# Kernel tuning notes

Measured on AMD Instinct MI355X. Metric: run time of the kernel, lower is better.

## Reference

```python
import jax, jax.numpy as jnp
import numpy as np

B, S, D, L = 2, 1024, 1024, 48
K = max(1, int(L * 0.1))  # = 4, matches torch k = max(1, int(num_paths * 0.1))
EPS = 1e-5  # torch LayerNorm default


def setup_inputs() -> dict:
    key = jax.random.key(0)
    ks = jax.random.split(key, 7)
    inv = 1.0 / np.sqrt(D).astype(np.float32)
    return {
        "x": jax.random.normal(ks[0], (B, S, D), jnp.float32),
        "gate_w": jax.random.normal(ks[1], (L, D), jnp.float32) * inv,          # gate_proj weight [L,D], no bias
        "lattice_weights": jax.random.normal(ks[2], (L, D, D), jnp.float32) * 0.02,
        "out_w": jax.random.normal(ks[3], (D, D), jnp.float32) * inv,            # out_proj weight [D,D]
        "out_b": jnp.zeros((D,), jnp.float32),
        "ln_g": jnp.ones((D,), jnp.float32),
        "ln_b": jnp.zeros((D,), jnp.float32),
    }


def reference(x, gate_w, lattice_weights, out_w, out_b, ln_g, ln_b):
    # Gate: top-k routing over L lattice paths
    logits = jnp.einsum('bsd,ld->bsl', x, gate_w)                 # [B,S,L]
    top_vals, idx = jax.lax.top_k(logits, K)                      # [B,S,K] each (descending, like torch.topk)
    scores = jax.nn.softmax(top_vals, axis=-1)                    # [B,S,K]

    # Mathematically identical to gathering [B,S,K,D,D] expert matrices and
    # weight-summing, but computed as one dense GEMM over all L experts
    # followed by a cheap gather -- avoids the 32GB intermediate.
    out_all = jnp.einsum('bsd,lde->bsle', x, lattice_weights)     # [B,S,L,D]
    sel = jnp.take_along_axis(out_all, idx[..., None], axis=2)    # [B,S,K,D]
    lattice_out = jnp.einsum('bskd,bsk->bsd', sel, scores)        # [B,S,D]

    y = x + jnp.einsum('bsd,ed->bse', lattice_out, out_w) + out_b # residual + out_proj
    mu = jnp.mean(y, axis=-1, keepdims=True)
    var = jnp.mean((y - mu) ** 2, axis=-1, keepdims=True)
    return ln_g * (y - mu) * jax.lax.rsqrt(var + EPS) + ln_b
```

## Files before the change

### kernel.cpp

```cpp
#include <hip/hip_runtime.h>
#include <stdint.h>

#define TT 2048
#define DD 1024
#define LL 48

typedef __attribute__((ext_vector_type(8))) short short8;
typedef __attribute__((ext_vector_type(4))) float f32x4;

static __device__ __forceinline__ unsigned int f2bf(float f) {
  union { float f; unsigned int u; } v; v.f = f;
  return (v.u + 0x7FFFu + ((v.u >> 16) & 1u)) >> 16;
}
static __device__ __forceinline__ unsigned int pack2(float a, float b) {
  return f2bf(a) | (f2bf(b) << 16);
}

__global__ __launch_bounds__(256) void k_gate(
    const float* __restrict__ x, const float* __restrict__ gw,
    unsigned short* __restrict__ xb,
    int* __restrict__ counts, int* __restrict__ btok, float* __restrict__ bscore)
{
  __shared__ float xs[8][1024];
  __shared__ float lg[8][48];
  const int tid = threadIdx.x;
  const int t0 = blockIdx.x * 8;
  for (int u = tid; u < 2048; u += 256) {
    int tok = u >> 8;
    int c = (u & 255) << 2;
    float4 v = *(const float4*)(x + (size_t)(t0 + tok) * DD + c);
    *(float4*)&xs[tok][c] = v;
    uint2 p; p.x = pack2(v.x, v.y); p.y = pack2(v.z, v.w);
    *(uint2*)(xb + (size_t)(t0 + tok) * DD + c) = p;
  }
  __syncthreads();
  const int lane = tid & 63, wid = tid >> 6;
  for (int li = 0; li < 12; ++li) {
    const int l = wid + (li << 2);
    const float4* gp = (const float4*)(gw + (size_t)l * DD);
    float4 g0 = gp[lane], g1 = gp[lane + 64], g2 = gp[lane + 128], g3 = gp[lane + 192];
    for (int tok = 0; tok < 8; ++tok) {
      const float4* xp = (const float4*)&xs[tok][0];
      float4 a0 = xp[lane], a1 = xp[lane + 64], a2 = xp[lane + 128], a3 = xp[lane + 192];
      float s = a0.x*g0.x + a0.y*g0.y + a0.z*g0.z + a0.w*g0.w
              + a1.x*g1.x + a1.y*g1.y + a1.z*g1.z + a1.w*g1.w
              + a2.x*g2.x + a2.y*g2.y + a2.z*g2.z + a2.w*g2.w
              + a3.x*g3.x + a3.y*g3.y + a3.z*g3.z + a3.w*g3.w;
      #pragma unroll
      for (int off = 32; off; off >>= 1) s += __shfl_down(s, off);
      if (lane == 0) lg[tok][l] = s;
    }
  }
  __syncthreads();
  if (tid < 8) {
    const int tok = tid;
    float v[4]; int id[4];
    unsigned long long taken = 0ull;
    for (int k = 0; k < 4; ++k) {
      float best = -3.4e38f; int bi = 0;
      for (int l = 0; l < 48; ++l) {
        float cand = lg[tok][l];
        if (!((taken >> l) & 1ull) && cand > best) { best = cand; bi = l; }
      }
      taken |= (1ull << bi); v[k] = best; id[k] = bi;
    }
    float e0 = 1.0f;
    float e1 = expf(v[1] - v[0]);
    float e2 = expf(v[2] - v[0]);
    float e3 = expf(v[3] - v[0]);
    float inv = 1.0f / (e0 + e1 + e2 + e3);
    float sc[4] = { e0*inv, e1*inv, e2*inv, e3*inv };
    for (int k = 0; k < 4; ++k) {
      int pos = atomicAdd(&counts[id[k]], 1);
      btok[id[k] * TT + pos] = ((t0 + tok) << 2) | k;
      bscore[id[k] * TT + pos] = sc[k];
    }
  }
}

__global__ __launch_bounds__(256, 2) void k_expert(
    const unsigned short* __restrict__ xb, const float* __restrict__ W,
    const int* __restrict__ counts, const int* __restrict__ btok,
    const float* __restrict__ bscore, float* __restrict__ sel)
{
  const int l = blockIdx.z;
  const int ncnt = counts[l];
  const int m0 = blockIdx.y * 256;
  if (m0 >= ncnt) return;
  const int n0 = blockIdx.x * 64;
  const int tid = threadIdx.x, lane = tid & 63, wid = tid >> 6;

  __shared__ alignas(16) unsigned short As[2][256][40];
  __shared__ alignas(16) unsigned short Bs[2][64][40];
  __shared__ int   toks[256];
  __shared__ float scs[256];

  {
    int r = m0 + tid;
    toks[tid] = (r < ncnt) ? btok[l * TT + r] : 0;
    scs[tid]  = (r < ncnt) ? bscore[l * TT + r] : 0.f;
  }
  __syncthreads();

  const int aq = tid >> 2, aseg = tid & 3;
  const size_t ra0 = (size_t)(toks[aq]       >> 2) * DD + aseg * 8;
  const size_t ra1 = (size_t)(toks[aq + 64]  >> 2) * DD + aseg * 8;
  const size_t ra2 = (size_t)(toks[aq + 128] >> 2) * DD + aseg * 8;
  const size_t ra3 = (size_t)(toks[aq + 192] >> 2) * DD + aseg * 8;
  const int be = tid >> 2, bks = tid & 3;
  const float* wb = W + (size_t)l * DD * DD + (size_t)(bks * 8) * DD + n0 + be;

  f32x4 acc[4][4];
  #pragma unroll
  for (int m = 0; m < 4; ++m)
    #pragma unroll
    for (int n = 0; n < 4; ++n)
      #pragma unroll
      for (int j = 0; j < 4; ++j) acc[m][n][j] = 0.f;

  int4 av0, av1, av2, av3;
  float wv[8];

#define E_LOAD(kk) do { \
    av0 = *(const int4*)(xb + ra0 + (kk)); \
    av1 = *(const int4*)(xb + ra1 + (kk)); \
    av2 = *(const int4*)(xb + ra2 + (kk)); \
    av3 = *(const int4*)(xb + ra3 + (kk)); \
    _Pragma("unroll") \
    for (int j = 0; j < 8; ++j) wv[j] = wb[(size_t)((kk) + j) * DD]; \
  } while (0)

#define E_STORE(b) do { \
    *(int4*)&As[b][aq][aseg * 8]       = av0; \
    *(int4*)&As[b][aq + 64][aseg * 8]  = av1; \
    *(int4*)&As[b][aq + 128][aseg * 8] = av2; \
    *(int4*)&As[b][aq + 192][aseg * 8] = av3; \
    uint4 pv; \
    pv.x = pack2(wv[0], wv[1]); pv.y = pack2(wv[2], wv[3]); \
    pv.z = pack2(wv[4], wv[5]); pv.w = pack2(wv[6], wv[7]); \
    *(uint4*)&Bs[b][be][bks * 8] = pv; \
  } while (0)

  E_LOAD(0); E_STORE(0); __syncthreads();
  int cur = 0;
  for (int t = 0; t < 32; ++t) {
    const bool more = (t < 31);
    if (more) E_LOAD((t + 1) * 32);
    short8 af[4], bf[4];
    #pragma unroll
    for (int n = 0; n < 4; ++n)
      bf[n] = *(const short8*)&Bs[cur][n * 16 + (lane & 15)][(lane >> 4) * 8];
    #pragma unroll
    for (int m = 0; m < 4; ++m)
      af[m] = *(const short8*)&As[cur][wid * 64 + m * 16 + (lane & 15)][(lane >> 4) * 8];
    #pragma unroll
    for (int m = 0; m < 4; ++m)
      #pragma unroll
      for (int n = 0; n < 4; ++n)
        acc[m][n] = __builtin_amdgcn_mfma_f32_16x16x32_bf16(af[m], bf[n], acc[m][n], 0, 0, 0);
    if (more) E_STORE(cur ^ 1);
    __syncthreads();
    cur ^= 1;
  }
#undef E_LOAD
#undef E_STORE

  #pragma unroll
  for (int m = 0; m < 4; ++m) {
    #pragma unroll
    for (int j = 0; j < 4; ++j) {
      const int r = wid * 64 + m * 16 + ((lane >> 4) << 2) + j;
      if (m0 + r < ncnt) {
        const float sc = scs[r];
        const size_t ob = (size_t)toks[r] * DD + n0 + (lane & 15);
        #pragma unroll
        for (int n = 0; n < 4; ++n)
          sel[ob + n * 16] = acc[m][n][j] * sc;
      }
    }
  }
}

__global__ __launch_bounds__(256) void k_combine(const float* __restrict__ sel,
                                                 unsigned short* __restrict__ lat)
{
  const size_t i = ((size_t)blockIdx.x * 256 + threadIdx.x) << 2;
  const size_t t = i >> 10, d = i & 1023;
  const float* p = sel + ((t << 2) << 10) + d;
  float4 s0 = *(const float4*)(p);
  float4 s1 = *(const float4*)(p + 1024);
  float4 s2 = *(const float4*)(p + 2048);
  float4 s3 = *(const float4*)(p + 3072);
  float r0 = s0.x + s1.x + s2.x + s3.x;
  float r1 = s0.y + s1.y + s2.y + s3.y;
  float r2 = s0.z + s1.z + s2.z + s3.z;
  float r3 = s0.w + s1.w + s2.w + s3.w;
  uint2 pk; pk.x = pack2(r0, r1); pk.y = pack2(r2, r3);
  *(uint2*)(lat + i) = pk;
}

__global__ __launch_bounds__(256, 2) void k_outproj(
    const unsigned short* __restrict__ lat, const float* __restrict__ W2,
    const float* __restrict__ xres, const float* __restrict__ bias,
    float* __restrict__ y)
{
  const int n0 = blockIdx.x * 64;
  const int m0 = blockIdx.y * 128;
  const int tid = threadIdx.x, lane = tid & 63, wid = tid >> 6;

  __shared__ alignas(16) unsigned short As[2][128][40];
  __shared__ alignas(16) unsigned short Bs[2][64][40];

  const int aq = tid >> 2, aseg = tid & 3;
  const unsigned short* la0 = lat + (size_t)(m0 + aq) * DD + aseg * 8;
  const unsigned short* la1 = lat + (size_t)(m0 + aq + 64) * DD + aseg * 8;
  const int be = tid >> 2, bks = tid & 3;
  const float* wb = W2 + (size_t)(n0 + be) * DD + bks * 8;

  f32x4 acc[2][4];
  #pragma unroll
  for (int m = 0; m < 2; ++m)
    #pragma unroll
    for (int n = 0; n < 4; ++n)
      #pragma unroll
      for (int j = 0; j < 4; ++j) acc[m][n][j] = 0.f;

  int4 av0, av1;
  float4 w0, w1;

#define O_LOAD(kk) do { \
    av0 = *(const int4*)(la0 + (kk)); \
    av1 = *(const int4*)(la1 + (kk)); \
    w0 = *(const float4*)(wb + (kk)); \
    w1 = *(const float4*)(wb + (kk) + 4); \
  } while (0)

#define O_STORE(b) do { \
    *(int4*)&As[b][aq][aseg * 8]      = av0; \
    *(int4*)&As[b][aq + 64][aseg * 8] = av1; \
    uint4 pv; \
    pv.x = pack2(w0.x, w0.y); pv.y = pack2(w0.z, w0.w); \
    pv.z = pack2(w1.x, w1.y); pv.w = pack2(w1.z, w1.w); \
    *(uint4*)&Bs[b][be][bks * 8] = pv; \
  } while (0)

  O_LOAD(0); O_STORE(0); __syncthreads();
  int cur = 0;
  for (int t = 0; t < 32; ++t) {
    const bool more = (t < 31);
    if (more) O_LOAD((t + 1) * 32);
    short8 af[2], bf[4];
    #pragma unroll
    for (int n = 0; n < 4; ++n)
      bf[n] = *(const short8*)&Bs[cur][n * 16 + (lane & 15)][(lane >> 4) * 8];
    #pragma unroll
    for (int m = 0; m < 2; ++m)
      af[m] = *(const short8*)&As[cur][wid * 32 + m * 16 + (lane & 15)][(lane >> 4) * 8];
    #pragma unroll
    for (int m = 0; m < 2; ++m)
      #pragma unroll
      for (int n = 0; n < 4; ++n)
        acc[m][n] = __builtin_amdgcn_mfma_f32_16x16x32_bf16(af[m], bf[n], acc[m][n], 0, 0, 0);
    if (more) O_STORE(cur ^ 1);
    __syncthreads();
    cur ^= 1;
  }
#undef O_LOAD
#undef O_STORE

  #pragma unroll
  for (int m = 0; m < 2; ++m) {
    #pragma unroll
    for (int j = 0; j < 4; ++j) {
      const int t = m0 + wid * 32 + m * 16 + ((lane >> 4) << 2) + j;
      #pragma unroll
      for (int n = 0; n < 4; ++n) {
        const int e = n0 + n * 16 + (lane & 15);
        y[(size_t)t * DD + e] = xres[(size_t)t * DD + e] + acc[m][n][j] + bias[e];
      }
    }
  }
}

__global__ __launch_bounds__(256) void k_ln(const float* __restrict__ y,
    const float* __restrict__ g, const float* __restrict__ b, float* __restrict__ out)
{
  const int t = blockIdx.x, tid = threadIdx.x;
  float4 v = *(const float4*)(y + (size_t)t * DD + tid * 4);
  float s  = v.x + v.y + v.z + v.w;
  float ss = v.x*v.x + v.y*v.y + v.z*v.z + v.w*v.w;
  #pragma unroll
  for (int off = 32; off; off >>= 1) { s += __shfl_down(s, off); ss += __shfl_down(ss, off); }
  __shared__ float rs[8];
  const int wid = tid >> 6, lane = tid & 63;
  if (lane == 0) { rs[wid] = s; rs[wid + 4] = ss; }
  __syncthreads();
  float S  = rs[0] + rs[1] + rs[2] + rs[3];
  float SS = rs[4] + rs[5] + rs[6] + rs[7];
  float mu = S * (1.0f / DD);
  float var = SS * (1.0f / DD) - mu * mu;
  float inv = rsqrtf(var + 1e-5f);
  float4 gg = *(const float4*)(g + tid * 4);
  float4 bb = *(const float4*)(b + tid * 4);
  float4 o;
  o.x = gg.x * (v.x - mu) * inv + bb.x;
  o.y = gg.y * (v.y - mu) * inv + bb.y;
  o.z = gg.z * (v.z - mu) * inv + bb.z;
  o.w = gg.w * (v.w - mu) * inv + bb.w;
  *(float4*)(out + (size_t)t * DD + tid * 4) = o;
}

extern "C" void kernel_launch(void* const* d_in, const int* in_sizes, int n_in,
                              void* d_out, int out_size, void* d_ws, size_t ws_size,
                              hipStream_t stream) {
  (void)in_sizes; (void)n_in; (void)out_size;
  const float* x   = (const float*)d_in[0];
  const float* gw  = (const float*)d_in[1];
  const float* lw  = (const float*)d_in[2];
  const float* ow  = (const float*)d_in[3];
  const float* obv = (const float*)d_in[4];
  const float* lng = (const float*)d_in[5];
  const float* lnb = (const float*)d_in[6];
  float* out = (float*)d_out;

  char* ws = (char*)d_ws;
  unsigned short* xb  = (unsigned short*)(ws);
  unsigned short* lat = (unsigned short*)(ws + (4u << 20));
  float* y            = (float*)(ws + (8u << 20));
  float* sel          = (float*)(ws + (16u << 20));
  int*   counts       = (int*)(ws + (48u << 20));
  int*   btok         = (int*)(ws + (48u << 20) + 4096);
  float* bscore       = (float*)(ws + (48u << 20) + 4096 + LL * TT * 4);
  if (ws_size < ((48u << 20) + 4096 + 2u * LL * TT * 4)) return;

  hipMemsetAsync(counts, 0, LL * sizeof(int), stream);
  k_gate<<<TT / 8, 256, 0, stream>>>(x, gw, xb, counts, btok, bscore);
  k_expert<<<dim3(16, 2, 48), 256, 0, stream>>>(xb, lw, counts, btok, bscore, sel);
  k_combine<<<TT * DD / (256 * 4), 256, 0, stream>>>(sel, lat);
  k_outproj<<<dim3(16, 16), 256, 0, stream>>>(lat, ow, x, obv, y);
  k_ln<<<TT, 256, 0, stream>>>(y, lng, lnb, out);
}
```

Baseline: 219.0 us.

## Pre-transpose expert weights to bf16 and use direct-to-LDS loads in expert GEMM

Adds a kernel that converts each call's fp32 lattice weights to a transposed bf16 layout using a swizzled shared-memory tile. A new expert GEMM then streams A and B tiles with global_load_lds into double-buffered, XOR-swizzled LDS and runs 128x128 tiles of bf16 MFMA, replacing the old kernel that read fp32 weights and converted them inside the GEMM loop. The new path runs only when the workspace is at least 133 MB; otherwise the old kernel is kept as a fallback. The conversion pass writes and re-reads an extra ~96 MB of bf16 weights every call, in exchange for a simpler, faster GEMM inner loop.

```diff
diff --git a/kernel.cpp b/kernel.cpp
--- a/kernel.cpp
+++ b/kernel.cpp
@@ -14,6 +14,12 @@
 }
 static __device__ __forceinline__ unsigned int pack2(float a, float b) {
   return f2bf(a) | (f2bf(b) << 16);
+}
+
+typedef __attribute__((address_space(1))) const void* as1_t;
+typedef __attribute__((address_space(3))) void* as3_t;
+static __device__ __forceinline__ void gll16(const void* g, void* s) {
+  __builtin_amdgcn_global_load_lds((as1_t)g, (as3_t)s, 16, 0, 0);
 }
 
 __global__ __launch_bounds__(256) void k_gate(
@@ -64,12 +70,11 @@
       }
       taken |= (1ull << bi); v[k] = best; id[k] = bi;
     }
-    float e0 = 1.0f;
     float e1 = expf(v[1] - v[0]);
     float e2 = expf(v[2] - v[0]);
     float e3 = expf(v[3] - v[0]);
-    float inv = 1.0f / (e0 + e1 + e2 + e3);
-    float sc[4] = { e0*inv, e1*inv, e2*inv, e3*inv };
+    float inv = 1.0f / (1.0f + e1 + e2 + e3);
+    float sc[4] = { inv, e1*inv, e2*inv, e3*inv };
     for (int k = 0; k < 4; ++k) {
       int pos = atomicAdd(&counts[id[k]], 1);
       btok[id[k] * TT + pos] = ((t0 + tok) << 2) | k;
@@ -78,7 +83,138 @@
   }
 }
 
-__global__ __launch_bounds__(256, 2) void k_expert(
+__global__ __launch_bounds__(256) void k_wconvT(const float* __restrict__ W,
+                                                unsigned short* __restrict__ Wt)
+{
+  const int l = blockIdx.z, d0 = blockIdx.y * 128, e0 = blockIdx.x * 128;
+  __shared__ unsigned short T[128][136];
+  const float* src = W + (size_t)l * DD * DD;
+  const int tid = threadIdx.x;
+  #pragma unroll
+  for (int i = 0; i < 16; ++i) {
+    int fl = i * 256 + tid;
+    int d = fl >> 5, e4 = fl & 31;
+    float4 v = *(const float4*)(src + (size_t)(d0 + d) * DD + e0 + e4 * 4);
+    #pragma unroll
+    for (int j = 0; j < 4; ++j) {
+      int e = e4 * 4 + j;
+      int unit = (d >> 3) ^ (e & 7);
+      float fv = (j == 0) ? v.x : (j == 1) ? v.y : (j == 2) ? v.z : v.w;
+      T[e][unit * 8 + (d & 7)] = (unsigned short)f2bf(fv);
+    }
+  }
+  __syncthreads();
+  #pragma unroll
+  for (int i2 = 0; i2 < 8; ++i2) {
+    int uo = i2 * 256 + tid;
+    int e = uo >> 4, ds = uo & 15;
+    short8 s8 = *(const short8*)&T[e][(ds ^ (e & 7)) * 8];
+    *(short8*)(Wt + ((size_t)l << 20) + (size_t)(e0 + e) * DD + d0 + ds * 8) = s8;
+  }
+}
+
+__global__ __launch_bounds__(256) void k_expert(
+    const unsigned short* __restrict__ xb, const unsigned short* __restrict__ Wt,
+    const int* __restrict__ counts, const int* __restrict__ btok,
+    const float* __restrict__ bscore, float* __restrict__ sel)
+{
+  const int l = blockIdx.z;
+  const int ncnt = counts[l];
+  const int m0 = blockIdx.y * 128;
+  if (m0 >= ncnt) return;
+  const int n0 = blockIdx.x * 128;
+  const int tid = threadIdx.x, lane = tid & 63, wid = tid >> 6;
+  const int wr = wid >> 1, wc = wid & 1;
+
+  __shared__ alignas(16) unsigned short As[2][128][64];
+  __shared__ alignas(16) unsigned short Bs[2][128][64];
+  __shared__ int   toks[128];
+  __shared__ float scs[128];
+
+  if (tid < 128) {
+    int r = m0 + tid;
+    toks[tid] = (r < ncnt) ? btok[l * TT + r] : 0;
+    scs[tid]  = (r < ncnt) ? bscore[l * TT + r] : 0.f;
+  }
+  __syncthreads();
+
+  const int rloc = tid >> 3;
+  const int sl = (tid & 7) ^ (rloc & 7);
+  const unsigned short* asrc[4];
+  const unsigned short* bsrc[4];
+  #pragma unroll
+  for (int i = 0; i < 4; ++i) {
+    int r = i * 32 + rloc;
+    asrc[i] = xb + (size_t)(toks[r] >> 2) * DD + sl * 8;
+    bsrc[i] = Wt + ((size_t)l << 20) + (size_t)(n0 + r) * DD + sl * 8;
+  }
+
+  f32x4 acc[4][4];
+  #pragma unroll
+  for (int m = 0; m < 4; ++m)
+    #pragma unroll
+    for (int n = 0; n < 4; ++n)
+      #pragma unroll
+      for (int j = 0; j < 4; ++j) acc[m][n][j] = 0.f;
+
+#define STAGE(buf, k0) do { \
+    unsigned short* ab = &As[buf][0][0]; \
+    unsigned short* bb = &Bs[buf][0][0]; \
+    _Pragma("unroll") \
+    for (int i = 0; i < 4; ++i) { \
+      gll16(asrc[i] + (k0), ab + (i * 256 + tid) * 8); \
+      gll16(bsrc[i] + (k0), bb + (i * 256 + tid) * 8); \
+    } \
+  } while (0)
+
+  const int fr = lane & 15, fq = lane >> 4, fswz = lane & 7;
+  const int slotk[2] = { fq ^ fswz, (4 + fq) ^ fswz };
+
+  STAGE(0, 0);
+  __syncthreads();
+  int cur = 0;
+  for (int t = 0; t < 16; ++t) {
+    if (t < 15) STAGE(cur ^ 1, (t + 1) * 64);
+    const unsigned short* Ab = &As[cur][0][0];
+    const unsigned short* Bb = &Bs[cur][0][0];
+    #pragma unroll
+    for (int kh = 0; kh < 2; ++kh) {
+      const int sA = slotk[kh];
+      short8 af[4], bf[4];
+      #pragma unroll
+      for (int m = 0; m < 4; ++m)
+        af[m] = *(const short8*)(Ab + ((wr * 64 + m * 16 + fr) << 6) + sA * 8);
+      #pragma unroll
+      for (int n = 0; n < 4; ++n)
+        bf[n] = *(const short8*)(Bb + ((wc * 64 + n * 16 + fr) << 6) + sA * 8);
+      #pragma unroll
+      for (int m = 0; m < 4; ++m)
+        #pragma unroll
+        for (int n = 0; n < 4; ++n)
+          acc[m][n] = __builtin_amdgcn_mfma_f32_16x16x32_bf16(af[m], bf[n], acc[m][n], 0, 0, 0);
+    }
+    __syncthreads();
+    cur ^= 1;
+  }
+#undef STAGE
+
+  #pragma unroll
+  for (int m = 0; m < 4; ++m) {
+    #pragma unroll
+    for (int j = 0; j < 4; ++j) {
+      const int r = wr * 64 + m * 16 + (fq << 2) + j;
+      if (m0 + r < ncnt) {
+        const float sc = scs[r];
+        const size_t ob = (size_t)toks[r] * DD + n0 + wc * 64 + fr;
+        #pragma unroll
+        for (int n = 0; n < 4; ++n)
+          sel[ob + n * 16] = acc[m][n][j] * sc;
+      }
+    }
+  }
+}
+
+__global__ __launch_bounds__(256, 2) void k_expert_fb(
     const unsigned short* __restrict__ xb, const float* __restrict__ W,
     const int* __restrict__ counts, const int* __restrict__ btok,
     const float* __restrict__ bscore, float* __restrict__ sel)
@@ -322,21 +458,42 @@
   const float* lng = (const float*)d_in[5];
   const float* lnb = (const float*)d_in[6];
   float* out = (float*)d_out;
-
   char* ws = (char*)d_ws;
-  unsigned short* xb  = (unsigned short*)(ws);
-  unsigned short* lat = (unsigned short*)(ws + (4u << 20));
-  float* y            = (float*)(ws + (8u << 20));
-  float* sel          = (float*)(ws + (16u << 20));
-  int*   counts       = (int*)(ws + (48u << 20));
-  int*   btok         = (int*)(ws + (48u << 20) + 4096);
-  float* bscore       = (float*)(ws + (48u << 20) + 4096 + LL * TT * 4);
-  if (ws_size < ((48u << 20) + 4096 + 2u * LL * TT * 4)) return;
-
-  hipMemsetAsync(counts, 0, LL * sizeof(int), stream);
-  k_gate<<<TT / 8, 256, 0, stream>>>(x, gw, xb, counts, btok, bscore);
-  k_expert<<<dim3(16, 2, 48), 256, 0, stream>>>(xb, lw, counts, btok, bscore, sel);
-  k_combine<<<TT * DD / (256 * 4), 256, 0, stream>>>(sel, lat);
-  k_outproj<<<dim3(16, 16), 256, 0, stream>>>(lat, ow, x, obv, y);
-  k_ln<<<TT, 256, 0, stream>>>(y, lng, lnb, out);
-}
+
+  const size_t NEED_NEW = (133ull << 20);
+  const size_t NEED_FB  = (48ull << 20) + 4096 + 2ull * LL * TT * 4;
+
+  if (ws_size >= NEED_NEW) {
+    float*          sel    = (float*)(ws);
+    unsigned short* xb     = (unsigned short*)(ws + (32ull << 20));
+    int*            counts = (int*)(ws + (36ull << 20));
+    int*            btok   = (int*)(ws + (36ull << 20) + 4096);
+    float*          bscore = (float*)(ws + (36ull << 20) + 4096 + (size_t)LL * TT * 4);
+    unsigned short* Wt     = (unsigned short*)(ws + (37ull << 20));
+    unsigned short* lat    = (unsigned short*)(ws + (37ull << 20));
+    float*          y      = (float*)(ws + (41ull << 20));
+
+    hipMemsetAsync(counts, 0, LL * sizeof(int), stream);
+    k_gate<<<TT / 8, 256, 0, stream>>>(x, gw, xb, counts, btok, bscore);
+    k_wconvT<<<dim3(8, 8, LL), 256, 0, stream>>>(lw, Wt);
+    k_expert<<<dim3(8, 2, LL), 256, 0, stream>>>(xb, Wt, counts, btok, bscore, sel);
+    k_combine<<<TT * DD / (256 * 4), 256, 0, stream>>>(sel, lat);
+    k_outproj<<<dim3(16, 16), 256, 0, stream>>>(lat, ow, x, obv, y);
+    k_ln<<<TT, 256, 0, stream>>>(y, lng, lnb, out);
+  } else if (ws_size >= NEED_FB) {
+    unsigned short* xb     = (unsigned short*)(ws);
+    unsigned short* lat    = (unsigned short*)(ws + (4ull << 20));
+    float*          y      = (float*)(ws + (8ull << 20));
+    float*          sel    = (float*)(ws + (16ull << 20));
+    int*            counts = (int*)(ws + (48ull << 20));
+    int*            btok   = (int*)(ws + (48ull << 20) + 4096);
+    float*          bscore = (float*)(ws + (48ull << 20) + 4096 + (size_t)LL * TT * 4);
+
+    hipMemsetAsync(counts, 0, LL * sizeof(int), stream);
+    k_gate<<<TT / 8, 256, 0, stream>>>(x, gw, xb, counts, btok, bscore);
+    k_expert_fb<<<dim3(16, 2, LL), 256, 0, stream>>>(xb, lw, counts, btok, bscore, sel);
+    k_combine<<<TT * DD / (256 * 4), 256, 0, stream>>>(sel, lat);
+    k_outproj<<<dim3(16, 16), 256, 0, stream>>>(lat, ow, x, obv, y);
+    k_ln<<<TT, 256, 0, stream>>>(y, lng, lnb, out);
+  }
+}
```

New measurement: 249.4 us. +13.9%, slower.

## Stage expert GEMM tiles via direct global-to-LDS loads with wider 512-thread tiles

Applied to the files above, without the earlier changes.

The expert GEMM now moves A (bf16 activations) and B (fp32 weights) straight into LDS with global_load_lds instead of going through registers, and converts the weights to bf16 when reading fragments out of LDS. The N tile doubles to 128 with 8 waves per block in a 4x2 arrangement, and the weight tile uses an XOR swizzle to avoid LDS bank conflicts. The aim is to drop register-staged copies and improve load overlap and weight reuse across the M tile. In exchange, fp32 weights take twice the LDS space and each MFMA fragment read now needs strided scalar LDS loads plus packing.

```diff
diff --git a/kernel.cpp b/kernel.cpp
--- a/kernel.cpp
+++ b/kernel.cpp
@@ -14,6 +14,12 @@
 }
 static __device__ __forceinline__ unsigned int pack2(float a, float b) {
   return f2bf(a) | (f2bf(b) << 16);
+}
+
+typedef __attribute__((address_space(1))) const void* as1_t;
+typedef __attribute__((address_space(3))) void* as3_t;
+static __device__ __forceinline__ void gll16(const void* g, void* s) {
+  __builtin_amdgcn_global_load_lds((as1_t)g, (as3_t)s, 16, 0, 0);
 }
 
 __global__ __launch_bounds__(256) void k_gate(
@@ -64,12 +70,11 @@
       }
       taken |= (1ull << bi); v[k] = best; id[k] = bi;
     }
-    float e0 = 1.0f;
     float e1 = expf(v[1] - v[0]);
     float e2 = expf(v[2] - v[0]);
     float e3 = expf(v[3] - v[0]);
-    float inv = 1.0f / (e0 + e1 + e2 + e3);
-    float sc[4] = { e0*inv, e1*inv, e2*inv, e3*inv };
+    float inv = 1.0f / (1.0f + e1 + e2 + e3);
+    float sc[4] = { inv, e1*inv, e2*inv, e3*inv };
     for (int k = 0; k < 4; ++k) {
       int pos = atomicAdd(&counts[id[k]], 1);
       btok[id[k] * TT + pos] = ((t0 + tok) << 2) | k;
@@ -78,7 +83,7 @@
   }
 }
 
-__global__ __launch_bounds__(256, 2) void k_expert(
+__global__ __launch_bounds__(512, 4) void k_expert(
     const unsigned short* __restrict__ xb, const float* __restrict__ W,
     const int* __restrict__ counts, const int* __restrict__ btok,
     const float* __restrict__ bscore, float* __restrict__ sel)
@@ -87,28 +92,29 @@
   const int ncnt = counts[l];
   const int m0 = blockIdx.y * 256;
   if (m0 >= ncnt) return;
-  const int n0 = blockIdx.x * 64;
+  const int n0 = blockIdx.x * 128;
   const int tid = threadIdx.x, lane = tid & 63, wid = tid >> 6;
-
-  __shared__ alignas(16) unsigned short As[2][256][40];
-  __shared__ alignas(16) unsigned short Bs[2][64][40];
+  const int wr = wid & 3, wc = wid >> 2;
+
+  __shared__ alignas(16) unsigned short As[2][256 * 32];
+  __shared__ alignas(16) float           Bs[2][32 * 128];
   __shared__ int   toks[256];
   __shared__ float scs[256];
 
-  {
+  if (tid < 256) {
     int r = m0 + tid;
     toks[tid] = (r < ncnt) ? btok[l * TT + r] : 0;
     scs[tid]  = (r < ncnt) ? bscore[l * TT + r] : 0.f;
   }
   __syncthreads();
 
-  const int aq = tid >> 2, aseg = tid & 3;
-  const size_t ra0 = (size_t)(toks[aq]       >> 2) * DD + aseg * 8;
-  const size_t ra1 = (size_t)(toks[aq + 64]  >> 2) * DD + aseg * 8;
-  const size_t ra2 = (size_t)(toks[aq + 128] >> 2) * DD + aseg * 8;
-  const size_t ra3 = (size_t)(toks[aq + 192] >> 2) * DD + aseg * 8;
-  const int be = tid >> 2, bks = tid & 3;
-  const float* wb = W + (size_t)l * DD * DD + (size_t)(bks * 8) * DD + n0 + be;
+  const unsigned short* asrc0 = xb + (size_t)(toks[tid >> 2]       >> 2) * DD + (tid & 3) * 8;
+  const unsigned short* asrc1 = xb + (size_t)(toks[128 + (tid >> 2)] >> 2) * DD + (tid & 3) * 8;
+  const float* Wl = W + (size_t)l * DD * DD + n0;
+  const int d0 = tid >> 5, cu = tid & 31;
+  const int d1 = d0 + 16;
+  const float* bsrc0 = Wl + (size_t)d0 * DD + ((cu ^ (((d0 >> 3) & 1) << 2)) << 2);
+  const float* bsrc1 = Wl + (size_t)d1 * DD + ((cu ^ (((d1 >> 3) & 1) << 2)) << 2);
 
   f32x4 acc[4][4];
   #pragma unroll
@@ -118,61 +124,55 @@
       #pragma unroll
       for (int j = 0; j < 4; ++j) acc[m][n][j] = 0.f;
 
-  int4 av0, av1, av2, av3;
-  float wv[8];
-
-#define E_LOAD(kk) do { \
-    av0 = *(const int4*)(xb + ra0 + (kk)); \
-    av1 = *(const int4*)(xb + ra1 + (kk)); \
-    av2 = *(const int4*)(xb + ra2 + (kk)); \
-    av3 = *(const int4*)(xb + ra3 + (kk)); \
-    _Pragma("unroll") \
-    for (int j = 0; j < 8; ++j) wv[j] = wb[(size_t)((kk) + j) * DD]; \
+#define STAGE(buf, k0) do { \
+    gll16(asrc0 + (k0), &As[buf][tid * 8]); \
+    gll16(asrc1 + (k0), &As[buf][(512 + tid) * 8]); \
+    gll16(bsrc0 + (size_t)(k0) * DD, &Bs[buf][tid * 4]); \
+    gll16(bsrc1 + (size_t)(k0) * DD, &Bs[buf][(512 + tid) * 4]); \
   } while (0)
 
-#define E_STORE(b) do { \
-    *(int4*)&As[b][aq][aseg * 8]       = av0; \
-    *(int4*)&As[b][aq + 64][aseg * 8]  = av1; \
-    *(int4*)&As[b][aq + 128][aseg * 8] = av2; \
-    *(int4*)&As[b][aq + 192][aseg * 8] = av3; \
-    uint4 pv; \
-    pv.x = pack2(wv[0], wv[1]); pv.y = pack2(wv[2], wv[3]); \
-    pv.z = pack2(wv[4], wv[5]); pv.w = pack2(wv[6], wv[7]); \
-    *(uint4*)&Bs[b][be][bks * 8] = pv; \
-  } while (0)
-
-  E_LOAD(0); E_STORE(0); __syncthreads();
+  const int fr = lane & 15, fq = lane >> 4;
+  const int bkey = (fq & 1) << 4;
+
+  STAGE(0, 0);
+  __syncthreads();
   int cur = 0;
   for (int t = 0; t < 32; ++t) {
-    const bool more = (t < 31);
-    if (more) E_LOAD((t + 1) * 32);
+    if (t < 31) STAGE(cur ^ 1, (t + 1) * 32);
+    const unsigned short* Ab = As[cur];
+    const float* Bb = Bs[cur];
     short8 af[4], bf[4];
     #pragma unroll
-    for (int n = 0; n < 4; ++n)
-      bf[n] = *(const short8*)&Bs[cur][n * 16 + (lane & 15)][(lane >> 4) * 8];
-    #pragma unroll
     for (int m = 0; m < 4; ++m)
-      af[m] = *(const short8*)&As[cur][wid * 64 + m * 16 + (lane & 15)][(lane >> 4) * 8];
+      af[m] = *(const short8*)(Ab + (wr * 64 + m * 16 + fr) * 32 + fq * 8);
+    #pragma unroll
+    for (int n = 0; n < 4; ++n) {
+      const float* bp = Bb + (size_t)fq * 8 * 128 + ((wc * 64 + n * 16 + fr) ^ bkey);
+      float w0 = bp[0],       w1 = bp[128],     w2 = bp[256],     w3 = bp[384];
+      float w4 = bp[512],     w5 = bp[640],     w6 = bp[768],     w7 = bp[896];
+      uint4 pv;
+      pv.x = pack2(w0, w1); pv.y = pack2(w2, w3);
+      pv.z = pack2(w4, w5); pv.w = pack2(w6, w7);
+      bf[n] = *(short8*)&pv;
+    }
     #pragma unroll
     for (int m = 0; m < 4; ++m)
       #pragma unroll
       for (int n = 0; n < 4; ++n)
         acc[m][n] = __builtin_amdgcn_mfma_f32_16x16x32_bf16(af[m], bf[n], acc[m][n], 0, 0, 0);
-    if (more) E_STORE(cur ^ 1);
     __syncthreads();
     cur ^= 1;
   }
-#undef E_LOAD
-#undef E_STORE
+#undef STAGE
 
   #pragma unroll
   for (int m = 0; m < 4; ++m) {
     #pragma unroll
     for (int j = 0; j < 4; ++j) {
-      const int r = wid * 64 + m * 16 + ((lane >> 4) << 2) + j;
+      const int r = wr * 64 + m * 16 + fq * 4 + j;
       if (m0 + r < ncnt) {
         const float sc = scs[r];
-        const size_t ob = (size_t)toks[r] * DD + n0 + (lane & 15);
+        const size_t ob = (size_t)toks[r] * DD + n0 + wc * 64 + fr;
         #pragma unroll
         for (int n = 0; n < 4; ++n)
           sel[ob + n * 16] = acc[m][n][j] * sc;
@@ -322,20 +322,20 @@
   const float* lng = (const float*)d_in[5];
   const float* lnb = (const float*)d_in[6];
   float* out = (float*)d_out;
-
   char* ws = (char*)d_ws;
-  unsigned short* xb  = (unsigned short*)(ws);
-  unsigned short* lat = (unsigned short*)(ws + (4u << 20));
-  float* y            = (float*)(ws + (8u << 20));
-  float* sel          = (float*)(ws + (16u << 20));
-  int*   counts       = (int*)(ws + (48u << 20));
-  int*   btok         = (int*)(ws + (48u << 20) + 4096);
-  float* bscore       = (float*)(ws + (48u << 20) + 4096 + LL * TT * 4);
-  if (ws_size < ((48u << 20) + 4096 + 2u * LL * TT * 4)) return;
+
+  unsigned short* xb     = (unsigned short*)(ws);
+  unsigned short* lat    = (unsigned short*)(ws + (4ull << 20));
+  float*          y      = (float*)(ws + (8ull << 20));
+  float*          sel    = (float*)(ws + (16ull << 20));
+  int*            counts = (int*)(ws + (48ull << 20));
+  int*            btok   = (int*)(ws + (48ull << 20) + 4096);
+  float*          bscore = (float*)(ws + (48ull << 20) + 4096 + (size_t)LL * TT * 4);
+  if (ws_size < ((48ull << 20) + 4096 + 2ull * LL * TT * 4)) return;
 
   hipMemsetAsync(counts, 0, LL * sizeof(int), stream);
   k_gate<<<TT / 8, 256, 0, stream>>>(x, gw, xb, counts, btok, bscore);
-  k_expert<<<dim3(16, 2, 48), 256, 0, stream>>>(xb, lw, counts, btok, bscore, sel);
+  k_expert<<<dim3(8, 2, LL), 512, 0, stream>>>(xb, lw, counts, btok, bscore, sel);
   k_combine<<<TT * DD / (256 * 4), 256, 0, stream>>>(sel, lat);
   k_outproj<<<dim3(16, 16), 256, 0, stream>>>(lat, ow, x, obv, y);
   k_ln<<<TT, 256, 0, stream>>>(y, lng, lnb, out);
```

Result: faster. 212.7 us (-2.9%).
